# Optimization experiments

Hardware: AMD Instinct MI355X
Metric: run time of the kernel (lower is better)

Reference implementation:

```python
import jax, jax.numpy as jnp
import numpy as np

N = 2048
D0, D1, D2 = 33, 33, 65
O = 128

def setup_inputs() -> dict:
    key = jax.random.key(0)
    k0, k1, k2, kw = jax.random.split(key, 4)
    x0 = jax.random.normal(k0, (N, D0), dtype=jnp.float32)
    x1 = jax.random.normal(k1, (N, D1), dtype=jnp.float32)
    x2 = jax.random.normal(k2, (N, D2), dtype=jnp.float32)
    # xavier_normal for weight_tensor of shape input_sizes + (output_size,):
    # fan_in = D0*D1*D2 treated as receptive field? torch xavier on 4D tensor uses
    # fan_in = shape[1]*receptive, but for faithfulness of *math* any gaussian init works;
    # use std = sqrt(2/(fan_in+fan_out)) with fan computed as torch does for >2D:
    # fan_in = shape[1]*shape[2]*shape[3]? torch: fan_in = size(1)*prod(size()[2:]),
    # fan_out = size(0)*prod(size()[2:]).
    recept = D2 * O
    fan_in = D1 * recept
    fan_out = D0 * recept
    std = float(np.sqrt(2.0 / (fan_in + fan_out)))
    weight_tensor = jax.random.normal(kw, (D0, D1, D2, O), dtype=jnp.float32) * std
    bias = jnp.zeros((O,), dtype=jnp.float32)
    return {"x0": x0, "x1": x1, "x2": x2, "weight_tensor": weight_tensor, "bias": bias}

def reference(x0, x1, x2, weight_tensor, bias):
    # fusion_tensor[n,a,b,c] = x0[n,a]*x1[n,b]*x2[n,c]  (chained outer products)
    # output[n,o] = sum_{a,b,c} fusion[n,a,b,c] * W[a,b,c,o] + bias; dropout(p=0) is identity.
    # Expressed as one fused einsum (same math, avoids HBM round-trip of the big intermediate).
    out = jnp.einsum('na,nb,nc,abco->no', x0, x1, x2, weight_tensor)
    out = jax.nn.relu(out + bias)
    return out
```

## Files before the change

kernel.cpp:

```cpp
#include <hip/hip_runtime.h>
#include <hip/hip_bf16.h>

typedef __attribute__((ext_vector_type(8))) short bf16x8;
typedef __attribute__((ext_vector_type(4))) float f32x4;

#define U_LD 2176
#define K_REAL 2145
#define NKT 34
#define DIM0 33
#define DIM1 33
#define DIM2 65
#define NROW 2048
#define OO 128

__device__ __forceinline__ unsigned short f2bf(float f) {
  union { float f; unsigned u; } v; v.f = f;
  unsigned r = v.u + 0x7fffu + ((v.u >> 16) & 1u);
  return (unsigned short)(r >> 16);
}

#define GLOAD_LDS16(SRC, DST) \
  __builtin_amdgcn_global_load_lds((const __attribute__((address_space(1))) void*)(SRC), \
                                   (__attribute__((address_space(3))) void*)(DST), 16, 0, 0)

__global__ __launch_bounds__(256) void prep_u_kernel(const float* __restrict__ x1,
                                                     const float* __restrict__ x2,
                                                     ushort* __restrict__ U) {
  __shared__ float s1[DIM1], s2[DIM2];
  int n = blockIdx.x;
  int tid = threadIdx.x;
  if (tid < DIM1) s1[tid] = x1[n * DIM1 + tid];
  int t2 = tid - DIM1;
  if (t2 >= 0 && t2 < DIM2) s2[t2] = x2[n * DIM2 + t2];
  __syncthreads();
  for (int k8 = tid; k8 < U_LD / 8; k8 += 256) {
    union { ushort us[8]; uint4 v; } pk;
#pragma unroll
    for (int j = 0; j < 8; ++j) {
      int k = k8 * 8 + j;
      float val = 0.f;
      if (k < K_REAL) { int b = k / DIM2; int c = k - b * DIM2; val = s1[b] * s2[c]; }
      pk.us[j] = f2bf(val);
    }
    *(uint4*)&U[(size_t)n * U_LD + k8 * 8] = pk.v;
  }
}

__global__ __launch_bounds__(256) void prep_wt_kernel(const float* __restrict__ W,
                                                      ushort* __restrict__ Wt) {
  __shared__ ushort s[64][130];
  int a = blockIdx.y;
  int k0 = blockIdx.x * 64;
  int tid = threadIdx.x;
  for (int idx = tid; idx < 64 * 32; idx += 256) {
    int kk = idx >> 5;
    int og = (idx & 31) * 4;
    int k = k0 + kk;
    float4 v = make_float4(0.f, 0.f, 0.f, 0.f);
    if (k < K_REAL) {
      int b = k / DIM2; int c = k - b * DIM2;
      v = *(const float4*)&W[(((size_t)a * DIM1 + b) * DIM2 + c) * OO + og];
    }
    s[kk][og]     = f2bf(v.x);
    s[kk][og + 1] = f2bf(v.y);
    s[kk][og + 2] = f2bf(v.z);
    s[kk][og + 3] = f2bf(v.w);
  }
  __syncthreads();
  int o  = tid >> 1;
  int kh = (tid & 1) * 32;
  union { ushort us[32]; uint4 v[4]; } pk;
#pragma unroll
  for (int j = 0; j < 32; ++j) pk.us[j] = s[kh + j][o];
  uint4* dst = (uint4*)&Wt[((size_t)a * OO + o) * U_LD + k0 + kh];
#pragma unroll
  for (int q = 0; q < 4; ++q) dst[q] = pk.v[q];
}

__global__ __launch_bounds__(256) void gemm_kernel(const ushort* __restrict__ U,
                                                   const ushort* __restrict__ Wt,
                                                   const float* __restrict__ x0,
                                                   float* __restrict__ out) {
  __shared__ ushort lds[2][12288];

  int tid = threadIdx.x;
  int lane = tid & 63;
  int w = tid >> 6;
  int wr = w >> 1, wc = w & 1;

  int orig = (int)blockIdx.x;
  int logical = (orig & 7) * 132 + (orig >> 3);
  int a = logical >> 5;
  int m = logical & 31;
  int n0 = m * 64;

  int kblk = lane >> 4;
  int r15 = lane & 15;
  int swz = lane & 7;

  f32x4 acc[2][4];
#pragma unroll
  for (int mi = 0; mi < 2; ++mi)
#pragma unroll
    for (int ni = 0; ni < 4; ++ni)
      acc[mi][ni] = (f32x4){0.f, 0.f, 0.f, 0.f};

  const ushort* WtA = Wt + (size_t)a * OO * U_LD;

  int c0 = tid;        int rA0 = c0 >> 3;  int dA0 = c0 * 8;
  int c1 = 256 + tid;  int rA1 = c1 >> 3;  int dA1 = c1 * 8;
  const ushort* pA0 = U + (size_t)(n0 + rA0) * U_LD + ((c0 & 7) ^ (rA0 & 7)) * 8;
  const ushort* pA1 = U + (size_t)(n0 + rA1) * U_LD + ((c1 & 7) ^ (rA1 & 7)) * 8;
  int cB0 = tid;        int rB0 = cB0 >> 3;  int dB0 = 4096 + cB0 * 8;
  int cB1 = 256 + tid;  int rB1 = cB1 >> 3;  int dB1 = 4096 + cB1 * 8;
  int cB2 = 512 + tid;  int rB2 = cB2 >> 3;  int dB2 = 4096 + cB2 * 8;
  int cB3 = 768 + tid;  int rB3 = cB3 >> 3;  int dB3 = 4096 + cB3 * 8;
  const ushort* pB0 = WtA + (size_t)rB0 * U_LD + ((cB0 & 7) ^ (rB0 & 7)) * 8;
  const ushort* pB1 = WtA + (size_t)rB1 * U_LD + ((cB1 & 7) ^ (rB1 & 7)) * 8;
  const ushort* pB2 = WtA + (size_t)rB2 * U_LD + ((cB2 & 7) ^ (rB2 & 7)) * 8;
  const ushort* pB3 = WtA + (size_t)rB3 * U_LD + ((cB3 & 7) ^ (rB3 & 7)) * 8;

  auto STAGE = [&](ushort* Lb) {
    GLOAD_LDS16(pA0, Lb + dA0); pA0 += 64;
    GLOAD_LDS16(pA1, Lb + dA1); pA1 += 64;
    GLOAD_LDS16(pB0, Lb + dB0); pB0 += 64;
    GLOAD_LDS16(pB1, Lb + dB1); pB1 += 64;
    GLOAD_LDS16(pB2, Lb + dB2); pB2 += 64;
    GLOAD_LDS16(pB3, Lb + dB3); pB3 += 64;
  };

  auto COMPUTE = [&](const ushort* Lb) {
    const char* base = (const char*)Lb;
#pragma unroll
    for (int ks = 0; ks < 2; ++ks) {
      bf16x8 af[2], bfr[4];
#pragma unroll
      for (int mi = 0; mi < 2; ++mi) {
        int off = (wr * 32 + mi * 16 + r15) * 128 + ((((ks * 4) + kblk) ^ swz) << 4);
        af[mi] = *(const bf16x8*)(base + off);
      }
#pragma unroll
      for (int ni = 0; ni < 4; ++ni) {
        int off = 8192 + (wc * 64 + ni * 16 + r15) * 128 + ((((ks * 4) + kblk) ^ swz) << 4);
        bfr[ni] = *(const bf16x8*)(base + off);
      }
      __builtin_amdgcn_s_setprio(1);
#pragma unroll
      for (int mi = 0; mi < 2; ++mi)
#pragma unroll
        for (int ni = 0; ni < 4; ++ni)
          acc[mi][ni] = __builtin_amdgcn_mfma_f32_16x16x32_bf16(af[mi], bfr[ni], acc[mi][ni], 0, 0, 0);
      __builtin_amdgcn_s_setprio(0);
    }
  };

  STAGE(&lds[0][0]);
  STAGE(&lds[1][0]);
  asm volatile("s_waitcnt vmcnt(6)" ::: "memory");
  __builtin_amdgcn_s_barrier();

  for (int it = 0; it < 16; ++it) {
    COMPUTE(&lds[0][0]);
    __builtin_amdgcn_s_barrier();
    STAGE(&lds[0][0]);
    asm volatile("s_waitcnt vmcnt(6)" ::: "memory");
    __builtin_amdgcn_s_barrier();
    COMPUTE(&lds[1][0]);
    __builtin_amdgcn_s_barrier();
    STAGE(&lds[1][0]);
    asm volatile("s_waitcnt vmcnt(6)" ::: "memory");
    __builtin_amdgcn_s_barrier();
  }
  COMPUTE(&lds[0][0]);
  asm volatile("s_waitcnt vmcnt(0)" ::: "memory");
  __builtin_amdgcn_s_barrier();
  COMPUTE(&lds[1][0]);

  int jrow = (lane >> 4) * 4;
#pragma unroll
  for (int mi = 0; mi < 2; ++mi) {
#pragma unroll
    for (int j = 0; j < 4; ++j) {
      int row = n0 + wr * 32 + mi * 16 + jrow + j;
      float s = x0[(size_t)row * DIM0 + a];
#pragma unroll
      for (int ni = 0; ni < 4; ++ni) {
        int col = wc * 64 + ni * 16 + r15;
        atomicAdd(&out[(size_t)row * OO + col], acc[mi][ni][j] * s);
      }
    }
  }
}

__global__ __launch_bounds__(256) void relu_kernel(float* __restrict__ out,
                                                   const float* __restrict__ bias) {
  int i = blockIdx.x * 256 + threadIdx.x;
  out[i] = fmaxf(out[i] + bias[i & (OO - 1)], 0.f);
}

extern "C" void kernel_launch(void* const* d_in, const int* in_sizes, int n_in,
                              void* d_out, int out_size, void* d_ws, size_t ws_size,
                              hipStream_t stream) {
  const float* x0   = (const float*)d_in[0];
  const float* x1   = (const float*)d_in[1];
  const float* x2   = (const float*)d_in[2];
  const float* W    = (const float*)d_in[3];
  const float* bias = (const float*)d_in[4];
  float* out = (float*)d_out;

  ushort* U  = (ushort*)d_ws;
  ushort* Wt = (ushort*)((char*)d_ws + (size_t)8912896);

  hipMemsetAsync(d_out, 0, (size_t)NROW * OO * sizeof(float), stream);
  prep_u_kernel<<<NROW, 256, 0, stream>>>(x1, x2, U);
  prep_wt_kernel<<<dim3(34, 33), 256, 0, stream>>>(W, Wt);
  gemm_kernel<<<1056, 256, 0, stream>>>(U, Wt, x0, out);
  relu_kernel<<<(NROW * OO) / 256, 256, 0, stream>>>(out, bias);
}
```

Baseline: 102.5 us.

## Enlarge GEMM tile to 128x128 and switch to 32x32x16 MFMA

The per-block M tile grows from 64 to 128 rows, so each block covers 128 rows by all 128 outputs for one value of a, and the grid halves to 528 blocks. The 16x16x32 MFMAs become 32x32x16 MFMAs with 16-element accumulators, and the LDS buffers grow to hold the larger A tile. The aim is more data reuse per LDS load, fewer redundant Wt fetches from global memory, and higher MFMA efficiency. The cost is more registers and LDS per block, fewer blocks to balance across the CUs, and a new epilogue row mapping for the atomics.

```diff
diff --git a/kernel.cpp b/kernel.cpp
--- a/kernel.cpp
+++ b/kernel.cpp
@@ -2,7 +2,7 @@
 #include <hip/hip_bf16.h>
 
 typedef __attribute__((ext_vector_type(8))) short bf16x8;
-typedef __attribute__((ext_vector_type(4))) float f32x4;
+typedef __attribute__((ext_vector_type(16))) float f32x16;
 
 #define U_LD 2176
 #define K_REAL 2145
@@ -77,11 +77,11 @@
   for (int q = 0; q < 4; ++q) dst[q] = pk.v[q];
 }
 
-__global__ __launch_bounds__(256) void gemm_kernel(const ushort* __restrict__ U,
-                                                   const ushort* __restrict__ Wt,
-                                                   const float* __restrict__ x0,
-                                                   float* __restrict__ out) {
-  __shared__ ushort lds[2][12288];
+__global__ __launch_bounds__(256, 2) void gemm_kernel(const ushort* __restrict__ U,
+                                                      const ushort* __restrict__ Wt,
+                                                      const float* __restrict__ x0,
+                                                      float* __restrict__ out) {
+  __shared__ ushort lds[2][16384];
 
   int tid = threadIdx.x;
   int lane = tid & 63;
@@ -89,86 +89,88 @@
   int wr = w >> 1, wc = w & 1;
 
   int orig = (int)blockIdx.x;
-  int logical = (orig & 7) * 132 + (orig >> 3);
-  int a = logical >> 5;
-  int m = logical & 31;
-  int n0 = m * 64;
-
-  int kblk = lane >> 4;
-  int r15 = lane & 15;
-  int swz = lane & 7;
-
-  f32x4 acc[2][4];
+  int logical = (orig & 7) * 66 + (orig >> 3);
+  int a = logical / 16;
+  int m = logical & 15;
+  int n0 = m * 128;
+
+  int r31 = lane & 31;
+  int ghi = lane >> 5;
+
+  f32x16 acc[2][2];
 #pragma unroll
   for (int mi = 0; mi < 2; ++mi)
 #pragma unroll
-    for (int ni = 0; ni < 4; ++ni)
-      acc[mi][ni] = (f32x4){0.f, 0.f, 0.f, 0.f};
+    for (int ni = 0; ni < 2; ++ni)
+      acc[mi][ni] = (f32x16){0.f,0.f,0.f,0.f,0.f,0.f,0.f,0.f,0.f,0.f,0.f,0.f,0.f,0.f,0.f,0.f};
 
   const ushort* WtA = Wt + (size_t)a * OO * U_LD;
 
-  int c0 = tid;        int rA0 = c0 >> 3;  int dA0 = c0 * 8;
-  int c1 = 256 + tid;  int rA1 = c1 >> 3;  int dA1 = c1 * 8;
-  const ushort* pA0 = U + (size_t)(n0 + rA0) * U_LD + ((c0 & 7) ^ (rA0 & 7)) * 8;
-  const ushort* pA1 = U + (size_t)(n0 + rA1) * U_LD + ((c1 & 7) ^ (rA1 & 7)) * 8;
-  int cB0 = tid;        int rB0 = cB0 >> 3;  int dB0 = 4096 + cB0 * 8;
-  int cB1 = 256 + tid;  int rB1 = cB1 >> 3;  int dB1 = 4096 + cB1 * 8;
-  int cB2 = 512 + tid;  int rB2 = cB2 >> 3;  int dB2 = 4096 + cB2 * 8;
-  int cB3 = 768 + tid;  int rB3 = cB3 >> 3;  int dB3 = 4096 + cB3 * 8;
-  const ushort* pB0 = WtA + (size_t)rB0 * U_LD + ((cB0 & 7) ^ (rB0 & 7)) * 8;
-  const ushort* pB1 = WtA + (size_t)rB1 * U_LD + ((cB1 & 7) ^ (rB1 & 7)) * 8;
-  const ushort* pB2 = WtA + (size_t)rB2 * U_LD + ((cB2 & 7) ^ (rB2 & 7)) * 8;
-  const ushort* pB3 = WtA + (size_t)rB3 * U_LD + ((cB3 & 7) ^ (rB3 & 7)) * 8;
+  const ushort* pA[4]; const ushort* pB[4];
+  int dA[4], dB[4];
+#pragma unroll
+  for (int i = 0; i < 4; ++i) {
+    int c = i * 256 + tid;
+    int row = c >> 3;
+    int ss = (c & 7) ^ (row & 7);
+    pA[i] = U + (size_t)(n0 + row) * U_LD + ss * 8;
+    dA[i] = c * 8;
+    pB[i] = WtA + (size_t)row * U_LD + ss * 8;
+    dB[i] = 8192 + c * 8;
+  }
 
   auto STAGE = [&](ushort* Lb) {
-    GLOAD_LDS16(pA0, Lb + dA0); pA0 += 64;
-    GLOAD_LDS16(pA1, Lb + dA1); pA1 += 64;
-    GLOAD_LDS16(pB0, Lb + dB0); pB0 += 64;
-    GLOAD_LDS16(pB1, Lb + dB1); pB1 += 64;
-    GLOAD_LDS16(pB2, Lb + dB2); pB2 += 64;
-    GLOAD_LDS16(pB3, Lb + dB3); pB3 += 64;
+#pragma unroll
+    for (int i = 0; i < 4; ++i) { GLOAD_LDS16(pA[i], Lb + dA[i]); pA[i] += 64; }
+#pragma unroll
+    for (int i = 0; i < 4; ++i) { GLOAD_LDS16(pB[i], Lb + dB[i]); pB[i] += 64; }
   };
 
   auto COMPUTE = [&](const ushort* Lb) {
     const char* base = (const char*)Lb;
-#pragma unroll
-    for (int ks = 0; ks < 2; ++ks) {
-      bf16x8 af[2], bfr[4];
-#pragma unroll
-      for (int mi = 0; mi < 2; ++mi) {
-        int off = (wr * 32 + mi * 16 + r15) * 128 + ((((ks * 4) + kblk) ^ swz) << 4);
-        af[mi] = *(const bf16x8*)(base + off);
-      }
-#pragma unroll
-      for (int ni = 0; ni < 4; ++ni) {
-        int off = 8192 + (wc * 64 + ni * 16 + r15) * 128 + ((((ks * 4) + kblk) ^ swz) << 4);
-        bfr[ni] = *(const bf16x8*)(base + off);
-      }
-      __builtin_amdgcn_s_setprio(1);
+    bf16x8 af[2][4], bfr[2][4];
+#pragma unroll
+    for (int mi = 0; mi < 2; ++mi) {
+      int row = wr * 64 + mi * 32 + r31;
+      int rb = row * 128, rs = row & 7;
+#pragma unroll
+      for (int ks = 0; ks < 4; ++ks)
+        af[mi][ks] = *(const bf16x8*)(base + rb + (((ks * 2 + ghi) ^ rs) << 4));
+    }
+#pragma unroll
+    for (int ni = 0; ni < 2; ++ni) {
+      int row = wc * 64 + ni * 32 + r31;
+      int rb = 16384 + row * 128, rs = row & 7;
+#pragma unroll
+      for (int ks = 0; ks < 4; ++ks)
+        bfr[ni][ks] = *(const bf16x8*)(base + rb + (((ks * 2 + ghi) ^ rs) << 4));
+    }
+    __builtin_amdgcn_s_setprio(1);
+#pragma unroll
+    for (int ks = 0; ks < 4; ++ks)
 #pragma unroll
       for (int mi = 0; mi < 2; ++mi)
 #pragma unroll
-        for (int ni = 0; ni < 4; ++ni)
-          acc[mi][ni] = __builtin_amdgcn_mfma_f32_16x16x32_bf16(af[mi], bfr[ni], acc[mi][ni], 0, 0, 0);
-      __builtin_amdgcn_s_setprio(0);
-    }
+        for (int ni = 0; ni < 2; ++ni)
+          acc[mi][ni] = __builtin_amdgcn_mfma_f32_32x32x16_bf16(af[mi][ks], bfr[ni][ks], acc[mi][ni], 0, 0, 0);
+    __builtin_amdgcn_s_setprio(0);
   };
 
   STAGE(&lds[0][0]);
   STAGE(&lds[1][0]);
-  asm volatile("s_waitcnt vmcnt(6)" ::: "memory");
+  asm volatile("s_waitcnt vmcnt(8)" ::: "memory");
   __builtin_amdgcn_s_barrier();
 
   for (int it = 0; it < 16; ++it) {
     COMPUTE(&lds[0][0]);
     __builtin_amdgcn_s_barrier();
     STAGE(&lds[0][0]);
-    asm volatile("s_waitcnt vmcnt(6)" ::: "memory");
+    asm volatile("s_waitcnt vmcnt(8)" ::: "memory");
     __builtin_amdgcn_s_barrier();
     COMPUTE(&lds[1][0]);
     __builtin_amdgcn_s_barrier();
     STAGE(&lds[1][0]);
-    asm volatile("s_waitcnt vmcnt(6)" ::: "memory");
+    asm volatile("s_waitcnt vmcnt(8)" ::: "memory");
     __builtin_amdgcn_s_barrier();
   }
   COMPUTE(&lds[0][0]);
@@ -176,17 +178,16 @@
   __builtin_amdgcn_s_barrier();
   COMPUTE(&lds[1][0]);
 
-  int jrow = (lane >> 4) * 4;
 #pragma unroll
   for (int mi = 0; mi < 2; ++mi) {
 #pragma unroll
-    for (int j = 0; j < 4; ++j) {
-      int row = n0 + wr * 32 + mi * 16 + jrow + j;
+    for (int r = 0; r < 16; ++r) {
+      int row = n0 + wr * 64 + mi * 32 + (r & 3) + 8 * (r >> 2) + 4 * ghi;
       float s = x0[(size_t)row * DIM0 + a];
 #pragma unroll
-      for (int ni = 0; ni < 4; ++ni) {
-        int col = wc * 64 + ni * 16 + r15;
-        atomicAdd(&out[(size_t)row * OO + col], acc[mi][ni][j] * s);
+      for (int ni = 0; ni < 2; ++ni) {
+        int col = wc * 64 + ni * 32 + r31;
+        atomicAdd(&out[(size_t)row * OO + col], acc[mi][ni][r] * s);
       }
     }
   }
@@ -214,6 +215,6 @@
   hipMemsetAsync(d_out, 0, (size_t)NROW * OO * sizeof(float), stream);
   prep_u_kernel<<<NROW, 256, 0, stream>>>(x1, x2, U);
   prep_wt_kernel<<<dim3(34, 33), 256, 0, stream>>>(W, Wt);
-  gemm_kernel<<<1056, 256, 0, stream>>>(U, Wt, x0, out);
+  gemm_kernel<<<528, 256, 0, stream>>>(U, Wt, x0, out);
   relu_kernel<<<(NROW * OO) / 256, 256, 0, stream>>>(out, bias);
 }
```

New measurement: 125.2 us. 22.1% more time.

## Enlarge GEMM M-tile to 128 rows and split K in half across blocks

Applied to the files above, without the earlier changes.

Each block of the per-a GEMM now covers 128 rows of U instead of 64, with a 4x4 MFMA accumulator tile per wave, and the K range is split into two halves handled by separate blocks. The grid stays at 1056 blocks, each doing 17 K-tiles instead of 34. The aim is to load each weight tile once per 128 rows and raise MFMA work per LDS byte. In exchange it doubles the atomic adds per output element, uses more registers and LDS per block, and adds launch_bounds occupancy hint 2.

```diff
diff --git a/kernel.cpp b/kernel.cpp
--- a/kernel.cpp
+++ b/kernel.cpp
@@ -7,6 +7,7 @@
 #define U_LD 2176
 #define K_REAL 2145
 #define NKT 34
+#define KSPLIT 17
 #define DIM0 33
 #define DIM1 33
 #define DIM2 65
@@ -77,11 +78,11 @@
   for (int q = 0; q < 4; ++q) dst[q] = pk.v[q];
 }
 
-__global__ __launch_bounds__(256) void gemm_kernel(const ushort* __restrict__ U,
-                                                   const ushort* __restrict__ Wt,
-                                                   const float* __restrict__ x0,
-                                                   float* __restrict__ out) {
-  __shared__ ushort lds[2][12288];
+__global__ __launch_bounds__(256, 2) void gemm_kernel(const ushort* __restrict__ U,
+                                                      const ushort* __restrict__ Wt,
+                                                      const float* __restrict__ x0,
+                                                      float* __restrict__ out) {
+  __shared__ ushort lds[2][16384];
 
   int tid = threadIdx.x;
   int lane = tid & 63;
@@ -91,62 +92,63 @@
   int orig = (int)blockIdx.x;
   int logical = (orig & 7) * 132 + (orig >> 3);
   int a = logical >> 5;
-  int m = logical & 31;
-  int n0 = m * 64;
+  int rem = logical & 31;
+  int m = rem >> 1;
+  int h = rem & 1;
+  int n0 = m * 128;
+  int kk0 = h * KSPLIT * 64;
 
   int kblk = lane >> 4;
   int r15 = lane & 15;
   int swz = lane & 7;
 
-  f32x4 acc[2][4];
-#pragma unroll
-  for (int mi = 0; mi < 2; ++mi)
+  f32x4 acc[4][4];
+#pragma unroll
+  for (int mi = 0; mi < 4; ++mi)
 #pragma unroll
     for (int ni = 0; ni < 4; ++ni)
       acc[mi][ni] = (f32x4){0.f, 0.f, 0.f, 0.f};
 
   const ushort* WtA = Wt + (size_t)a * OO * U_LD;
 
-  int c0 = tid;        int rA0 = c0 >> 3;  int dA0 = c0 * 8;
-  int c1 = 256 + tid;  int rA1 = c1 >> 3;  int dA1 = c1 * 8;
-  const ushort* pA0 = U + (size_t)(n0 + rA0) * U_LD + ((c0 & 7) ^ (rA0 & 7)) * 8;
-  const ushort* pA1 = U + (size_t)(n0 + rA1) * U_LD + ((c1 & 7) ^ (rA1 & 7)) * 8;
-  int cB0 = tid;        int rB0 = cB0 >> 3;  int dB0 = 4096 + cB0 * 8;
-  int cB1 = 256 + tid;  int rB1 = cB1 >> 3;  int dB1 = 4096 + cB1 * 8;
-  int cB2 = 512 + tid;  int rB2 = cB2 >> 3;  int dB2 = 4096 + cB2 * 8;
-  int cB3 = 768 + tid;  int rB3 = cB3 >> 3;  int dB3 = 4096 + cB3 * 8;
-  const ushort* pB0 = WtA + (size_t)rB0 * U_LD + ((cB0 & 7) ^ (rB0 & 7)) * 8;
-  const ushort* pB1 = WtA + (size_t)rB1 * U_LD + ((cB1 & 7) ^ (rB1 & 7)) * 8;
-  const ushort* pB2 = WtA + (size_t)rB2 * U_LD + ((cB2 & 7) ^ (rB2 & 7)) * 8;
-  const ushort* pB3 = WtA + (size_t)rB3 * U_LD + ((cB3 & 7) ^ (rB3 & 7)) * 8;
+  const ushort* pA[4]; const ushort* pB[4];
+  int dA[4], dB[4];
+#pragma unroll
+  for (int i = 0; i < 4; ++i) {
+    int c = i * 256 + tid;
+    int row = c >> 3;
+    int ss = (c & 7) ^ (row & 7);
+    pA[i] = U + (size_t)(n0 + row) * U_LD + kk0 + ss * 8;
+    dA[i] = c * 8;
+    pB[i] = WtA + (size_t)row * U_LD + kk0 + ss * 8;
+    dB[i] = 8192 + c * 8;
+  }
 
   auto STAGE = [&](ushort* Lb) {
-    GLOAD_LDS16(pA0, Lb + dA0); pA0 += 64;
-    GLOAD_LDS16(pA1, Lb + dA1); pA1 += 64;
-    GLOAD_LDS16(pB0, Lb + dB0); pB0 += 64;
-    GLOAD_LDS16(pB1, Lb + dB1); pB1 += 64;
-    GLOAD_LDS16(pB2, Lb + dB2); pB2 += 64;
-    GLOAD_LDS16(pB3, Lb + dB3); pB3 += 64;
+#pragma unroll
+    for (int i = 0; i < 4; ++i) { GLOAD_LDS16(pA[i], Lb + dA[i]); pA[i] += 64; }
+#pragma unroll
+    for (int i = 0; i < 4; ++i) { GLOAD_LDS16(pB[i], Lb + dB[i]); pB[i] += 64; }
   };
 
   auto COMPUTE = [&](const ushort* Lb) {
     const char* base = (const char*)Lb;
 #pragma unroll
     for (int ks = 0; ks < 2; ++ks) {
-      bf16x8 af[2], bfr[4];
-#pragma unroll
-      for (int mi = 0; mi < 2; ++mi) {
-        int off = (wr * 32 + mi * 16 + r15) * 128 + ((((ks * 4) + kblk) ^ swz) << 4);
+      bf16x8 af[4], bfr[4];
+#pragma unroll
+      for (int mi = 0; mi < 4; ++mi) {
+        int off = (wr * 64 + mi * 16 + r15) * 128 + ((((ks * 4) + kblk) ^ swz) << 4);
         af[mi] = *(const bf16x8*)(base + off);
       }
 #pragma unroll
       for (int ni = 0; ni < 4; ++ni) {
-        int off = 8192 + (wc * 64 + ni * 16 + r15) * 128 + ((((ks * 4) + kblk) ^ swz) << 4);
+        int off = 16384 + (wc * 64 + ni * 16 + r15) * 128 + ((((ks * 4) + kblk) ^ swz) << 4);
         bfr[ni] = *(const bf16x8*)(base + off);
       }
       __builtin_amdgcn_s_setprio(1);
 #pragma unroll
-      for (int mi = 0; mi < 2; ++mi)
+      for (int mi = 0; mi < 4; ++mi)
 #pragma unroll
         for (int ni = 0; ni < 4; ++ni)
           acc[mi][ni] = __builtin_amdgcn_mfma_f32_16x16x32_bf16(af[mi], bfr[ni], acc[mi][ni], 0, 0, 0);
@@ -156,32 +158,37 @@
 
   STAGE(&lds[0][0]);
   STAGE(&lds[1][0]);
-  asm volatile("s_waitcnt vmcnt(6)" ::: "memory");
-  __builtin_amdgcn_s_barrier();
-
-  for (int it = 0; it < 16; ++it) {
+  asm volatile("s_waitcnt vmcnt(8)" ::: "memory");
+  __builtin_amdgcn_s_barrier();
+
+  for (int it = 0; it < 7; ++it) {
     COMPUTE(&lds[0][0]);
     __builtin_amdgcn_s_barrier();
     STAGE(&lds[0][0]);
-    asm volatile("s_waitcnt vmcnt(6)" ::: "memory");
+    asm volatile("s_waitcnt vmcnt(8)" ::: "memory");
     __builtin_amdgcn_s_barrier();
     COMPUTE(&lds[1][0]);
     __builtin_amdgcn_s_barrier();
     STAGE(&lds[1][0]);
-    asm volatile("s_waitcnt vmcnt(6)" ::: "memory");
+    asm volatile("s_waitcnt vmcnt(8)" ::: "memory");
     __builtin_amdgcn_s_barrier();
   }
   COMPUTE(&lds[0][0]);
+  __builtin_amdgcn_s_barrier();
+  STAGE(&lds[0][0]);
+  asm volatile("s_waitcnt vmcnt(8)" ::: "memory");
+  __builtin_amdgcn_s_barrier();
+  COMPUTE(&lds[1][0]);
   asm volatile("s_waitcnt vmcnt(0)" ::: "memory");
   __builtin_amdgcn_s_barrier();
-  COMPUTE(&lds[1][0]);
+  COMPUTE(&lds[0][0]);
 
   int jrow = (lane >> 4) * 4;
 #pragma unroll
-  for (int mi = 0; mi < 2; ++mi) {
+  for (int mi = 0; mi < 4; ++mi) {
 #pragma unroll
     for (int j = 0; j < 4; ++j) {
-      int row = n0 + wr * 32 + mi * 16 + jrow + j;
+      int row = n0 + wr * 64 + mi * 16 + jrow + j;
       float s = x0[(size_t)row * DIM0 + a];
 #pragma unroll
       for (int ni = 0; ni < 4; ++ni) {
```

New measurement: 129.0 us. 1.26x slower.

## Enlarge GEMM tile to 128x128 with 512-thread blocks for more weight reuse

Applied to the files above, without the earlier changes.

Each GEMM block now covers 128 rows instead of 64 and runs 8 waves. The weight tile for a given slice is therefore loaded once per 128 rows, halving its global traffic, and the grid is halved to 528 blocks. LDS per block grows to 64 KB double-buffered and the vmcnt waits are adjusted to four loads per stage. Fewer blocks and the larger LDS footprint may reduce occupancy and tail balance across CUs.

```diff
diff --git a/kernel.cpp b/kernel.cpp
--- a/kernel.cpp
+++ b/kernel.cpp
@@ -77,11 +77,11 @@
   for (int q = 0; q < 4; ++q) dst[q] = pk.v[q];
 }
 
-__global__ __launch_bounds__(256) void gemm_kernel(const ushort* __restrict__ U,
-                                                   const ushort* __restrict__ Wt,
-                                                   const float* __restrict__ x0,
-                                                   float* __restrict__ out) {
-  __shared__ ushort lds[2][12288];
+__global__ __launch_bounds__(512, 4) void gemm_kernel(const ushort* __restrict__ U,
+                                                      const ushort* __restrict__ Wt,
+                                                      const float* __restrict__ x0,
+                                                      float* __restrict__ out) {
+  __shared__ ushort lds[2][16384];
 
   int tid = threadIdx.x;
   int lane = tid & 63;
@@ -89,10 +89,10 @@
   int wr = w >> 1, wc = w & 1;
 
   int orig = (int)blockIdx.x;
-  int logical = (orig & 7) * 132 + (orig >> 3);
-  int a = logical >> 5;
-  int m = logical & 31;
-  int n0 = m * 64;
+  int logical = (orig & 7) * 66 + (orig >> 3);
+  int a = logical >> 4;
+  int m = logical & 15;
+  int n0 = m * 128;
 
   int kblk = lane >> 4;
   int r15 = lane & 15;
@@ -107,26 +107,24 @@
 
   const ushort* WtA = Wt + (size_t)a * OO * U_LD;
 
-  int c0 = tid;        int rA0 = c0 >> 3;  int dA0 = c0 * 8;
-  int c1 = 256 + tid;  int rA1 = c1 >> 3;  int dA1 = c1 * 8;
-  const ushort* pA0 = U + (size_t)(n0 + rA0) * U_LD + ((c0 & 7) ^ (rA0 & 7)) * 8;
-  const ushort* pA1 = U + (size_t)(n0 + rA1) * U_LD + ((c1 & 7) ^ (rA1 & 7)) * 8;
-  int cB0 = tid;        int rB0 = cB0 >> 3;  int dB0 = 4096 + cB0 * 8;
-  int cB1 = 256 + tid;  int rB1 = cB1 >> 3;  int dB1 = 4096 + cB1 * 8;
-  int cB2 = 512 + tid;  int rB2 = cB2 >> 3;  int dB2 = 4096 + cB2 * 8;
-  int cB3 = 768 + tid;  int rB3 = cB3 >> 3;  int dB3 = 4096 + cB3 * 8;
-  const ushort* pB0 = WtA + (size_t)rB0 * U_LD + ((cB0 & 7) ^ (rB0 & 7)) * 8;
-  const ushort* pB1 = WtA + (size_t)rB1 * U_LD + ((cB1 & 7) ^ (rB1 & 7)) * 8;
-  const ushort* pB2 = WtA + (size_t)rB2 * U_LD + ((cB2 & 7) ^ (rB2 & 7)) * 8;
-  const ushort* pB3 = WtA + (size_t)rB3 * U_LD + ((cB3 & 7) ^ (rB3 & 7)) * 8;
+  const ushort* pA[2]; const ushort* pB[2];
+  int dA[2], dB[2];
+#pragma unroll
+  for (int i = 0; i < 2; ++i) {
+    int c = i * 512 + tid;
+    int row = c >> 3;
+    int ss = (c & 7) ^ (row & 7);
+    pA[i] = U + (size_t)(n0 + row) * U_LD + ss * 8;
+    dA[i] = c * 8;
+    pB[i] = WtA + (size_t)row * U_LD + ss * 8;
+    dB[i] = 8192 + c * 8;
+  }
 
   auto STAGE = [&](ushort* Lb) {
-    GLOAD_LDS16(pA0, Lb + dA0); pA0 += 64;
-    GLOAD_LDS16(pA1, Lb + dA1); pA1 += 64;
-    GLOAD_LDS16(pB0, Lb + dB0); pB0 += 64;
-    GLOAD_LDS16(pB1, Lb + dB1); pB1 += 64;
-    GLOAD_LDS16(pB2, Lb + dB2); pB2 += 64;
-    GLOAD_LDS16(pB3, Lb + dB3); pB3 += 64;
+#pragma unroll
+    for (int i = 0; i < 2; ++i) { GLOAD_LDS16(pA[i], Lb + dA[i]); pA[i] += 64; }
+#pragma unroll
+    for (int i = 0; i < 2; ++i) { GLOAD_LDS16(pB[i], Lb + dB[i]); pB[i] += 64; }
   };
 
   auto COMPUTE = [&](const ushort* Lb) {
@@ -141,7 +139,7 @@
       }
 #pragma unroll
       for (int ni = 0; ni < 4; ++ni) {
-        int off = 8192 + (wc * 64 + ni * 16 + r15) * 128 + ((((ks * 4) + kblk) ^ swz) << 4);
+        int off = 16384 + (wc * 64 + ni * 16 + r15) * 128 + ((((ks * 4) + kblk) ^ swz) << 4);
         bfr[ni] = *(const bf16x8*)(base + off);
       }
       __builtin_amdgcn_s_setprio(1);
@@ -156,19 +154,19 @@
 
   STAGE(&lds[0][0]);
   STAGE(&lds[1][0]);
-  asm volatile("s_waitcnt vmcnt(6)" ::: "memory");
+  asm volatile("s_waitcnt vmcnt(4)" ::: "memory");
   __builtin_amdgcn_s_barrier();
 
   for (int it = 0; it < 16; ++it) {
     COMPUTE(&lds[0][0]);
     __builtin_amdgcn_s_barrier();
     STAGE(&lds[0][0]);
-    asm volatile("s_waitcnt vmcnt(6)" ::: "memory");
+    asm volatile("s_waitcnt vmcnt(4)" ::: "memory");
     __builtin_amdgcn_s_barrier();
     COMPUTE(&lds[1][0]);
     __builtin_amdgcn_s_barrier();
     STAGE(&lds[1][0]);
-    asm volatile("s_waitcnt vmcnt(6)" ::: "memory");
+    asm volatile("s_waitcnt vmcnt(4)" ::: "memory");
     __builtin_amdgcn_s_barrier();
   }
   COMPUTE(&lds[0][0]);
@@ -214,6 +212,6 @@
   hipMemsetAsync(d_out, 0, (size_t)NROW * OO * sizeof(float), stream);
   prep_u_kernel<<<NROW, 256, 0, stream>>>(x1, x2, U);
   prep_wt_kernel<<<dim3(34, 33), 256, 0, stream>>>(W, Wt);
-  gemm_kernel<<<1056, 256, 0, stream>>>(U, Wt, x0, out);
+  gemm_kernel<<<528, 512, 0, stream>>>(U, Wt, x0, out);
   relu_kernel<<<(NROW * OO) / 256, 256, 0, stream>>>(out, bias);
 }
```

Result: slower. 110.8 us (+8.1%).
